# Performance work log

Measured on AMD Instinct MI355X. Metric: run time of the kernel, lower is better.

## Reference

```python
import jax, jax.numpy as jnp
import numpy as np

B, L, E, F, H, V = 64, 32, 512, 512, 1024, 10000


def setup_inputs() -> dict:
    key = jax.random.key(0)
    ks = jax.random.split(key, 20)
    def lin_w(k, out_d, in_d):
        # 4 stacked gate weights (i, f, o, c), PyTorch Linear-style scale
        s = 1.0 / np.sqrt(in_d)
        return jax.random.uniform(k, (4, out_d, in_d), jnp.float32, -s, s)
    def lin_b(k, out_d, in_d):
        s = 1.0 / np.sqrt(in_d)
        return jax.random.uniform(k, (4, out_d), jnp.float32, -s, s)
    inp = {
        "captions": jax.random.randint(ks[0], (B, L), 0, V),
        "image_features": jax.random.normal(ks[1], (B, E), jnp.float32),
        "B_emb": jax.random.normal(ks[2], (V, E), jnp.float32),
        "V_W": lin_w(ks[3], F, E), "V_b": lin_b(ks[4], F, E),
        "S_W": lin_w(ks[5], F, F), "S_b": lin_b(ks[6], F, F),
        "U_W": lin_w(ks[7], H, F), "U_b": lin_b(ks[8], H, F),
        "W_W": lin_w(ks[9], H, H), "W_b": lin_b(ks[10], H, H),
        "C_W": jax.random.uniform(ks[11], (V, H), jnp.float32, -1.0/np.sqrt(H), 1.0/np.sqrt(H)),
        "C_b": jax.random.uniform(ks[12], (V,), jnp.float32, -1.0/np.sqrt(H), 1.0/np.sqrt(H)),
        # original uses nn.init.uniform_ on fresh tensors -> U[0,1)
        "h0": jax.random.uniform(ks[13], (B, H), jnp.float32),
        "c0": jax.random.uniform(ks[14], (B, H), jnp.float32),
    }
    return inp


def reference(captions, image_features, B_emb, V_W, V_b, S_W, S_b, U_W, U_b,
              W_W, W_b, C_W, C_b, h0, c0):
    emb = B_emb[captions]                                   # [B, L, E]
    embedded = jnp.concatenate([image_features[:, None, :], emb], axis=1)  # [B, L+1, E]
    x = embedded[:, :-1, :]                                 # [B, T, E], T = L
    # input-dependent gate pre-activations (V -> S_d[mode] -> U), independent of h
    g = jnp.einsum('bte,gfe->btgf', x, V_W) + V_b           # [B, T, 4, F]
    g = jnp.einsum('btgf,gof->btgo', g, S_W) + S_b          # [B, T, 4, F]
    g = jnp.einsum('btgf,ghf->btgh', g, U_W) + U_b          # [B, T, 4, H]

    def step(carry, g_t):
        h, c = carry
        hg = jnp.einsum('bk,ghk->bgh', h, W_W) + W_b        # [B, 4, H]
        z = g_t + hg
        i_t = jax.nn.sigmoid(z[:, 0])
        f_t = jax.nn.sigmoid(z[:, 1])
        o_t = jax.nn.sigmoid(z[:, 2])
        c_tilda = jnp.tanh(z[:, 3])
        c_new = f_t * c + i_t * c_tilda
        h_new = o_t * c_new
        logits = h_new @ C_W.T + C_b                        # [B, V]
        return (h_new, c_new), logits

    _, outs = jax.lax.scan(step, (h0, c0), jnp.swapaxes(g, 0, 1))  # outs: [T, B, V]
    return jnp.swapaxes(outs, 0, 1)                         # [B, T, V]
```

## Files before the change

kernel.cpp:

```cpp
#include <hip/hip_runtime.h>
#include <hip/hip_bf16.h>

typedef __attribute__((ext_vector_type(8))) __bf16 bf16x8;
typedef __attribute__((ext_vector_type(4))) float f32x4;
typedef unsigned short ushort_t;

#define Bdim 64
#define Tdim 32
#define Edim 512
#define Fdim 512
#define Hdim 1024
#define Vdim 10000
#define SCAN_BLOCKS 64
#define CONS_BLOCKS 157

__device__ __forceinline__ float bf2f(ushort_t u) {
    unsigned int x = ((unsigned int)u) << 16;
    union { unsigned int i; float f; } c; c.i = x; return c.f;
}
__device__ __forceinline__ ushort_t f2bf(float f) {
    __hip_bfloat16 h = __float2bfloat16(f);
    union { __hip_bfloat16 h; ushort_t u; } c; c.h = h; return c.u;
}

__device__ __forceinline__ void gload_lds16(const void* g, void* l) {
    __builtin_amdgcn_global_load_lds(
        (const __attribute__((address_space(1))) unsigned int*)g,
        (__attribute__((address_space(3))) unsigned int*)l, 16, 0, 0);
}

__device__ __forceinline__ void store_short_wt(ushort_t* p, ushort_t v) {
    asm volatile("global_store_short %0, %1, off sc0 sc1"
                 : : "v"(p), "v"((unsigned int)v) : "memory");
}
__device__ __forceinline__ void store_uint_wt(unsigned int* p, unsigned int v) {
    asm volatile("global_store_dword %0, %1, off sc0 sc1"
                 : : "v"(p), "v"(v) : "memory");
}

__global__ void cvt_all(const float* __restrict__ vw, const float* __restrict__ sw,
                        const float* __restrict__ uw, const float* __restrict__ ww,
                        const float* __restrict__ cw, const float* __restrict__ h0,
                        ushort_t* __restrict__ mir, unsigned int* __restrict__ flg) {
    if (blockIdx.x == 0) {
        int4 zz = {0, 0, 0, 0};
        ((int4*)flg)[threadIdx.x * 2 + 0] = zz;
        ((int4*)flg)[threadIdx.x * 2 + 1] = zz;
    }
    long idx = ((long)blockIdx.x * blockDim.x + threadIdx.x) * 8;
    const float* src; long off;
    if      (idx <  1048576L) { src = vw; off = idx; }
    else if (idx <  2097152L) { src = sw; off = idx - 1048576L; }
    else if (idx <  4194304L) { src = uw; off = idx - 2097152L; }
    else if (idx <  8388608L) { src = ww; off = idx - 4194304L; }
    else if (idx < 18628608L) { src = cw; off = idx - 8388608L; }
    else if (idx < 18694144L) { src = h0; off = idx - 18628608L; }
    else return;
    float4 a = *(const float4*)(src + off);
    float4 b = *(const float4*)(src + off + 4);
    ushort_t o[8];
    o[0] = f2bf(a.x); o[1] = f2bf(a.y); o[2] = f2bf(a.z); o[3] = f2bf(a.w);
    o[4] = f2bf(b.x); o[5] = f2bf(b.y); o[6] = f2bf(b.z); o[7] = f2bf(b.w);
    *(int4*)(mir + idx) = *(const int4*)o;
}

__global__ void build_x(const int* __restrict__ cap,
                        const float* __restrict__ img,
                        const float* __restrict__ emb,
                        ushort_t* __restrict__ X) {
    int idx = blockIdx.x * blockDim.x + threadIdx.x;
    int row = idx >> 6;
    int c8  = (idx & 63) << 3;
    int b = row >> 5, t = row & 31;
    const float* src = (t == 0) ? (img + (size_t)b * Edim)
                                : (emb + (size_t)cap[b * Tdim + (t - 1)] * Edim);
    float4 a  = *(const float4*)(src + c8);
    float4 bb = *(const float4*)(src + c8 + 4);
    ushort_t o[8];
    o[0] = f2bf(a.x);  o[1] = f2bf(a.y);  o[2] = f2bf(a.z);  o[3] = f2bf(a.w);
    o[4] = f2bf(bb.x); o[5] = f2bf(bb.y); o[6] = f2bf(bb.z); o[7] = f2bf(bb.w);
    *(int4*)(X + (size_t)row * Edim + c8) = *(const int4*)o;
}

__launch_bounds__(256)
__global__ void gemm_bt(const ushort_t* __restrict__ A, long lda, long gsA,
                        const ushort_t* __restrict__ Bm, long ldb, long gsB,
                        void* __restrict__ Cv, long ldc, long gsC,
                        const float* __restrict__ bias, long gsBias,
                        int N, int K, int f32out, int zpack, int aswap) {
    __shared__ ushort_t As[128 * 64];
    __shared__ ushort_t Bs[128 * 64];
    int z = blockIdx.z;
    A += (size_t)z * gsA; Bm += (size_t)z * gsB; bias += (size_t)z * gsBias;

    int nx = gridDim.x, ny = gridDim.y;
    int lin = blockIdx.x + nx * blockIdx.y;
    int per_xcd = (nx * ny) >> 3;
    int l2 = (lin & 7) * per_xcd + (lin >> 3);
    int bx = l2 / ny, by = l2 % ny;

    int tid = threadIdx.x;
    int w = tid >> 6, l = tid & 63;
    int wm = (w >> 1) * 64, wn = (w & 1) * 64;
    int m0 = by * 128, n0 = bx * 128;

    int srow = tid >> 3;
    int scol = (tid & 7) << 3;

    int lane_r = l & 15;
    int lane_k = (l >> 4) << 3;

    f32x4 zero = {0.f, 0.f, 0.f, 0.f};
    f32x4 acc[4][4];
#pragma unroll
    for (int i = 0; i < 4; i++)
#pragma unroll
        for (int j = 0; j < 4; j++) acc[i][j] = zero;

    for (int k0 = 0; k0 < K; k0 += 64) {
#pragma unroll
        for (int j = 0; j < 4; j++) {
            int r = srow + j * 32;
            int pr = m0 + r;
            if (aswap) pr = ((pr & 31) << 6) + (pr >> 5);
            int sc = scol ^ ((r & 7) << 3);
            gload_lds16(A + (size_t)pr * lda + k0 + sc, &As[r * 64 + scol]);
        }
#pragma unroll
        for (int j = 0; j < 4; j++) {
            int r = srow + j * 32;
            int br = n0 + r; if (br > N - 1) br = N - 1;
            int sc = scol ^ ((r & 7) << 3);
            gload_lds16(Bm + (size_t)br * ldb + k0 + sc, &Bs[r * 64 + scol]);
        }
        __syncthreads();
#pragma unroll
        for (int kk = 0; kk < 64; kk += 32) {
            bf16x8 af[4], bfr[4];
#pragma unroll
            for (int i = 0; i < 4; i++) {
                int ar = wm + i * 16 + lane_r;
                af[i] = *(const bf16x8*)&As[ar * 64 + ((kk + lane_k) ^ ((ar & 7) << 3))];
            }
#pragma unroll
            for (int j = 0; j < 4; j++) {
                int br2 = wn + j * 16 + lane_r;
                bfr[j] = *(const bf16x8*)&Bs[br2 * 64 + ((kk + lane_k) ^ ((br2 & 7) << 3))];
            }
#pragma unroll
            for (int i = 0; i < 4; i++)
#pragma unroll
                for (int j = 0; j < 4; j++)
                    acc[i][j] = __builtin_amdgcn_mfma_f32_16x16x32_bf16(af[i], bfr[j], acc[i][j], 0, 0, 0);
        }
        __syncthreads();
    }

    int row_base = m0 + wm + ((l >> 4) << 2);
    int col_base = n0 + wn + lane_r;
#pragma unroll
    for (int j = 0; j < 4; j++) {
        int col = col_base + j * 16;
        if (col < N) {
            float bv = bias[col];
#pragma unroll
            for (int i = 0; i < 4; i++) {
#pragma unroll
                for (int r = 0; r < 4; r++) {
                    int row = row_base + i * 16 + r;
                    float v = acc[i][j][r] + bv;
                    if (zpack) {
                        int b = row >> 5, tt = row & 31;
                        size_t idx = (((size_t)(tt * 64 + (col >> 4)) * 4 + z) * 16
                                      + (col & 15)) * 64 + b;
                        ((ushort_t*)Cv)[idx] = f2bf(v);
                    } else if (f32out) {
                        ((float*)Cv)[(size_t)z * gsC + (size_t)row * ldc + col] = v;
                    } else {
                        ((ushort_t*)Cv)[(size_t)z * gsC + (size_t)row * ldc + col] = f2bf(v);
                    }
                }
            }
        }
    }
}

#define GLD(i, o) asm volatile("global_load_dwordx4 %0, %1, off offset:" o \
                               : "=v"(ab[i]) : "v"(apx))
#define CHUNK(d, n, ISSUE)                                                                   \
    do {                                                                                     \
        const int kc2 = ((d) * 32 + lane_kb) * 2;                                            \
        bf16x8 b0 = *(const bf16x8*)((const char*)Ws + ((     lane_r) * 2048 + (kc2 ^ swz)));\
        bf16x8 b1 = *(const bf16x8*)((const char*)Ws + ((16 + lane_r) * 2048 + (kc2 ^ swz)));\
        bf16x8 b2 = *(const bf16x8*)((const char*)Ws + ((32 + lane_r) * 2048 + (kc2 ^ swz)));\
        bf16x8 b3 = *(const bf16x8*)((const char*)Ws + ((48 + lane_r) * 2048 + (kc2 ^ swz)));\
        asm volatile("s_waitcnt vmcnt(" n ")");                                              \
        __builtin_amdgcn_sched_barrier(0);                                                   \
        bf16x8 av = __builtin_bit_cast(bf16x8, ab[(d) & 15]);                                \
        acc[0] = __builtin_amdgcn_mfma_f32_16x16x32_bf16(av, b0, acc[0], 0, 0, 0);           \
        acc[1] = __builtin_amdgcn_mfma_f32_16x16x32_bf16(av, b1, acc[1], 0, 0, 0);           \
        acc[2] = __builtin_amdgcn_mfma_f32_16x16x32_bf16(av, b2, acc[2], 0, 0, 0);           \
        acc[3] = __builtin_amdgcn_mfma_f32_16x16x32_bf16(av, b3, acc[3], 0, 0, 0);           \
        ISSUE;                                                                               \
    } while (0)
#define KLOOP32()                                                                            \
    int4 ab[16];                                                                             \
    GLD(0, "0");    GLD(1, "64");   GLD(2, "128");  GLD(3, "192");                           \
    GLD(4, "256");  GLD(5, "320");  GLD(6, "384");  GLD(7, "448");                           \
    GLD(8, "512");  GLD(9, "576");  GLD(10, "640"); GLD(11, "704");                          \
    GLD(12, "768"); GLD(13, "832"); GLD(14, "896"); GLD(15, "960");                          \
    CHUNK(0, "15", GLD(0, "1024"));  CHUNK(1, "15", GLD(1, "1088"));                         \
    CHUNK(2, "15", GLD(2, "1152"));  CHUNK(3, "15", GLD(3, "1216"));                         \
    CHUNK(4, "15", GLD(4, "1280"));  CHUNK(5, "15", GLD(5, "1344"));                         \
    CHUNK(6, "15", GLD(6, "1408"));  CHUNK(7, "15", GLD(7, "1472"));                         \
    CHUNK(8, "15", GLD(8, "1536"));  CHUNK(9, "15", GLD(9, "1600"));                         \
    CHUNK(10, "15", GLD(10, "1664")); CHUNK(11, "15", GLD(11, "1728"));                      \
    CHUNK(12, "15", GLD(12, "1792")); CHUNK(13, "15", GLD(13, "1856"));                      \
    CHUNK(14, "15", GLD(14, "1920")); CHUNK(15, "15", GLD(15, "1984"));                      \
    CHUNK(16, "15", (void)0); CHUNK(17, "14", (void)0);                                      \
    CHUNK(18, "13", (void)0); CHUNK(19, "12", (void)0);                                      \
    CHUNK(20, "11", (void)0); CHUNK(21, "10", (void)0);                                      \
    CHUNK(22, "9", (void)0);  CHUNK(23, "8", (void)0);                                       \
    CHUNK(24, "7", (void)0);  CHUNK(25, "6", (void)0);                                       \
    CHUNK(26, "5", (void)0);  CHUNK(27, "4", (void)0);                                       \
    CHUNK(28, "3", (void)0);  CHUNK(29, "2", (void)0);                                       \
    CHUNK(30, "1", (void)0);  CHUNK(31, "0", (void)0)

__launch_bounds__(256, 1)
__global__ void lstm_fused(const ushort_t* __restrict__ Wm,
                           const float* __restrict__ Wb,
                           const ushort_t* __restrict__ zb,
                           const ushort_t* __restrict__ h0b,
                           const float* __restrict__ c0,
                           ushort_t* __restrict__ Hbt,
                           unsigned int* __restrict__ flags,
                           const ushort_t* __restrict__ CWb,
                           const float* __restrict__ Cb,
                           float* __restrict__ out) {
    __shared__ ushort_t Ws[64 * 1024];
    int bid = blockIdx.x;
    int tid = threadIdx.x;
    int w = tid >> 6, l = tid & 63;
    int lane_r = l & 15, lane_kb = (l >> 4) << 3;

    if (bid < SCAN_BLOCKS) {
        int cg = bid;
        for (int e = tid * 8; e < 65536; e += 2048) {
            int rowl = e >> 10, ke = e & 1023;
            int g = rowl >> 4, hc = rowl & 15;
            const ushort_t* src = Wm + ((size_t)(g * Hdim + cg * 16 + hc)) * Hdim + ke;
            int dstb = rowl * 2048 + ((ke * 2) ^ ((rowl & 7) << 4));
            *(int4*)((char*)Ws + dstb) = *(const int4*)src;
        }
        int hcol = cg * 16 + lane_r;
        float wbv[4];
#pragma unroll
        for (int g = 0; g < 4; g++) wbv[g] = Wb[g * Hdim + hcol];
        int rb0 = w * 16 + ((l >> 4) << 2);
        float cst[4];
#pragma unroll
        for (int r = 0; r < 4; r++) cst[r] = c0[(size_t)(rb0 + r) * Hdim + hcol];
        __syncthreads();

        int arow = w * 16 + lane_r;
        int swz = (lane_r & 7) << 4;

        for (int t = 0; t < Tdim; t++) {
            ushort_t g3s[4][4];
            size_t zbase = ((size_t)t * 64 + cg) * 4096 + (size_t)lane_r * 64 + rb0;
#pragma unroll
            for (int g = 0; g < 4; g++)
                *(ushort4*)g3s[g] = *(const ushort4*)(zb + zbase + (size_t)g * 1024);

            if (t > 0) {
                const unsigned int* fp = flags + (size_t)(t - 1) * 64 + l;
                unsigned int v;
                do {
                    v = __hip_atomic_load(fp, __ATOMIC_RELAXED, __HIP_MEMORY_SCOPE_AGENT);
                } while (__ballot(v != 0) != 0xFFFFFFFFFFFFFFFFull);
            }
            __builtin_amdgcn_sched_barrier(0);

            const ushort_t* hp = t ? (Hbt + (size_t)(t - 1) * (Bdim * Hdim)) : h0b;
            const ushort_t* apx = hp + (size_t)arow * Hdim + lane_kb;

            f32x4 zero = {0.f, 0.f, 0.f, 0.f};
            f32x4 acc[4];
#pragma unroll
            for (int g = 0; g < 4; g++) acc[g] = zero;

            KLOOP32();

#pragma unroll
            for (int r = 0; r < 4; r++) {
                float zi = acc[0][r] + wbv[0] + bf2f(g3s[0][r]);
                float zf = acc[1][r] + wbv[1] + bf2f(g3s[1][r]);
                float zo = acc[2][r] + wbv[2] + bf2f(g3s[2][r]);
                float zc = acc[3][r] + wbv[3] + bf2f(g3s[3][r]);
                float it = __builtin_amdgcn_rcpf(1.f + __expf(-zi));
                float ft = __builtin_amdgcn_rcpf(1.f + __expf(-zf));
                float ot = __builtin_amdgcn_rcpf(1.f + __expf(-zo));
                float e2 = __expf(-2.f * zc);
                float ct = (1.f - e2) * __builtin_amdgcn_rcpf(1.f + e2);
                float cn = ft * cst[r] + it * ct;
                cst[r] = cn;
                store_short_wt(Hbt + (size_t)t * (Bdim * Hdim) + (size_t)(rb0 + r) * Hdim + hcol,
                               f2bf(ot * cn));
            }

            asm volatile("s_waitcnt vmcnt(0)" ::: "memory");
            __syncthreads();
            if (tid == 0) store_uint_wt(flags + (size_t)t * 64 + cg, 1u);
        }
    } else {
        int j = bid - SCAN_BLOCKS;
        for (int e = tid * 8; e < 65536; e += 2048) {
            int rowl = e >> 10, ke = e & 1023;
            int n = j * 64 + rowl; if (n > Vdim - 1) n = Vdim - 1;
            const ushort_t* src = CWb + (size_t)n * Hdim + ke;
            int dstb = rowl * 2048 + ((ke * 2) ^ ((rowl & 7) << 4));
            *(int4*)((char*)Ws + dstb) = *(const int4*)src;
        }
        int rb0 = w * 16 + ((l >> 4) << 2);
        int arow = w * 16 + lane_r;
        int swz = (lane_r & 7) << 4;
        float cbv[4];
#pragma unroll
        for (int g = 0; g < 4; g++) {
            int col = j * 64 + g * 16 + lane_r;
            cbv[g] = Cb[col > Vdim - 1 ? Vdim - 1 : col];
        }
        __syncthreads();

        for (int t = 0; t < Tdim; t++) {
            if (w == 0) {
                const unsigned int* fp = flags + (size_t)t * 64 + l;
                unsigned int v;
                do {
                    __builtin_amdgcn_s_sleep(8);
                    v = __hip_atomic_load(fp, __ATOMIC_RELAXED, __HIP_MEMORY_SCOPE_AGENT);
                } while (__ballot(v != 0) != 0xFFFFFFFFFFFFFFFFull);
            }
            __syncthreads();
            __builtin_amdgcn_sched_barrier(0);

            const ushort_t* apx = Hbt + (size_t)t * (Bdim * Hdim) + (size_t)arow * Hdim + lane_kb;

            f32x4 zero = {0.f, 0.f, 0.f, 0.f};
            f32x4 acc[4];
#pragma unroll
            for (int g = 0; g < 4; g++) acc[g] = zero;

            KLOOP32();

#pragma unroll
            for (int g = 0; g < 4; g++) {
                int col = j * 64 + g * 16 + lane_r;
                if (col < Vdim) {
#pragma unroll
                    for (int r = 0; r < 4; r++)
                        out[((size_t)(rb0 + r) * Tdim + t) * Vdim + col] = acc[g][r] + cbv[g];
                }
            }
        }
    }
}

extern "C" void kernel_launch(void* const* d_in, const int* in_sizes, int n_in,
                              void* d_out, int out_size, void* d_ws, size_t ws_size,
                              hipStream_t stream) {
    const int*   cap  = (const int*)d_in[0];
    const float* img  = (const float*)d_in[1];
    const float* Bemb = (const float*)d_in[2];
    const float* V_W  = (const float*)d_in[3];
    const float* V_b  = (const float*)d_in[4];
    const float* S_W  = (const float*)d_in[5];
    const float* S_b  = (const float*)d_in[6];
    const float* U_W  = (const float*)d_in[7];
    const float* U_b  = (const float*)d_in[8];
    const float* W_W  = (const float*)d_in[9];
    const float* W_b  = (const float*)d_in[10];
    const float* C_W  = (const float*)d_in[11];
    const float* C_b  = (const float*)d_in[12];
    const float* h0   = (const float*)d_in[13];
    const float* c0   = (const float*)d_in[14];

    char* ws = (char*)d_ws;
    int fused = ws_size >= (size_t)(64u) * 1024 * 1024;

    ushort_t* mir = (ushort_t*)(ws);
    ushort_t* X   = (ushort_t*)(ws + (size_t)(36u << 20));
    ushort_t* g1  = (ushort_t*)(ws + (size_t)(38u << 20));
    ushort_t *g2, *Hbt, *zbp; unsigned int* flags;
    if (fused) {
        zbp   = (ushort_t*)(ws + (size_t)(36u << 20));
        g2    = (ushort_t*)(ws + (size_t)(52u << 20));
        Hbt   = (ushort_t*)(ws + (size_t)(60u << 20));
        flags = (unsigned int*)(ws + (size_t)(36u << 20) - 16384);
    } else {
        zbp   = (ushort_t*)d_out;
        g2    = (ushort_t*)(ws + (size_t)(46u << 20));
        Hbt   = (ushort_t*)(ws + (size_t)(54u << 20));
        flags = (unsigned int*)(ws + (size_t)(58u << 20));
    }

    const ushort_t* V_Wb = mir;
    const ushort_t* S_Wb = mir + 1048576L;
    const ushort_t* U_Wb = mir + 2097152L;
    const ushort_t* W_Wb = mir + 4194304L;
    const ushort_t* C_Wb = mir + 8388608L;
    const ushort_t* h0b  = mir + 18628608L;

    cvt_all<<<9128, 256, 0, stream>>>(V_W, S_W, U_W, W_W, C_W, h0, mir, flags);
    build_x<<<512, 256, 0, stream>>>(cap, img, Bemb, X);

    gemm_bt<<<dim3(16, 16, 1), 256, 0, stream>>>(X, 512, 0, V_Wb, 512, 0,
                                                 g1, 2048, 0, V_b, 0, 2048, 512, 0, 0, 0);
    gemm_bt<<<dim3(4, 16, 4), 256, 0, stream>>>(g1, 2048, 512, S_Wb, 512, 512 * 512,
                                                g2, 2048, 512, S_b, 512, 512, 512, 0, 0, 0);
    gemm_bt<<<dim3(8, 16, 4), 256, 0, stream>>>(g2, 2048, 512, U_Wb, 512, 1024 * 512,
                                                zbp, 0, 0, U_b, 1024, 1024, 512, 0, 1, 0);
    {
        const ushort_t* a0 = W_Wb; const float* a1 = W_b; const ushort_t* a2 = zbp;
        const ushort_t* a3 = h0b;  const float* a4 = c0;  ushort_t* a5 = Hbt;
        unsigned int* a6 = flags;  const ushort_t* a7 = C_Wb; const float* a8 = C_b;
        float* a9 = (float*)d_out;
        void* sargs[10] = {(void*)&a0, (void*)&a1, (void*)&a2, (void*)&a3, (void*)&a4,
                           (void*)&a5, (void*)&a6, (void*)&a7, (void*)&a8, (void*)&a9};
        int grid = fused ? (SCAN_BLOCKS + CONS_BLOCKS) : SCAN_BLOCKS;
        hipLaunchCooperativeKernel((const void*)lstm_fused, dim3(grid), dim3(256),
                                   sargs, 0, stream);
    }
    if (!fused) {
        gemm_bt<<<dim3(79, 16, 1), 256, 0, stream>>>(Hbt, 1024, 0, C_Wb, 1024, 0,
                                                     d_out, 10000, 0, C_b, 0,
                                                     10000, 1024, 1, 0, 1);
    }
}
```

Baseline: 381.5 us.

## Convert C_W to bf16 inside fused consumer blocks and use single done flag

In the fused path the vocabulary projection weights are no longer converted to bf16 by the pre-pass kernel. Each consumer block now loads its fp32 slice of C_W and converts it while filling shared memory, which shrinks cvt_all and removes the extra global write and re-read of the bf16 mirror. Consumers also stop polling all 64 per-block flags and instead spin on one per-step 'done' word, written by scan block 0 after it sees all flags for that step. This cuts polling traffic but adds one hop of latency before consumers start each step.

```diff
diff --git a/kernel.cpp b/kernel.cpp
--- a/kernel.cpp
+++ b/kernel.cpp
@@ -40,12 +40,12 @@
 
 __global__ void cvt_all(const float* __restrict__ vw, const float* __restrict__ sw,
                         const float* __restrict__ uw, const float* __restrict__ ww,
-                        const float* __restrict__ cw, const float* __restrict__ h0,
+                        const float* __restrict__ h0, const float* __restrict__ cw,
                         ushort_t* __restrict__ mir, unsigned int* __restrict__ flg) {
     if (blockIdx.x == 0) {
         int4 zz = {0, 0, 0, 0};
-        ((int4*)flg)[threadIdx.x * 2 + 0] = zz;
-        ((int4*)flg)[threadIdx.x * 2 + 1] = zz;
+#pragma unroll
+        for (int q = 0; q < 4; q++) ((int4*)flg)[threadIdx.x * 4 + q] = zz;
     }
     long idx = ((long)blockIdx.x * blockDim.x + threadIdx.x) * 8;
     const float* src; long off;
@@ -53,8 +53,8 @@
     else if (idx <  2097152L) { src = sw; off = idx - 1048576L; }
     else if (idx <  4194304L) { src = uw; off = idx - 2097152L; }
     else if (idx <  8388608L) { src = ww; off = idx - 4194304L; }
-    else if (idx < 18628608L) { src = cw; off = idx - 8388608L; }
-    else if (idx < 18694144L) { src = h0; off = idx - 18628608L; }
+    else if (idx <  8454144L) { src = h0; off = idx - 8388608L; }
+    else if (idx < 18694144L) { src = cw; off = idx - 8454144L; }
     else return;
     float4 a = *(const float4*)(src + off);
     float4 b = *(const float4*)(src + off + 4);
@@ -234,10 +234,11 @@
                            const float* __restrict__ c0,
                            ushort_t* __restrict__ Hbt,
                            unsigned int* __restrict__ flags,
-                           const ushort_t* __restrict__ CWb,
+                           const float* __restrict__ CWf,
                            const float* __restrict__ Cb,
                            float* __restrict__ out) {
     __shared__ ushort_t Ws[64 * 1024];
+    unsigned int* done = flags + 2048;
     int bid = blockIdx.x;
     int tid = threadIdx.x;
     int w = tid >> 6, l = tid & 63;
@@ -278,6 +279,7 @@
                 do {
                     v = __hip_atomic_load(fp, __ATOMIC_RELAXED, __HIP_MEMORY_SCOPE_AGENT);
                 } while (__ballot(v != 0) != 0xFFFFFFFFFFFFFFFFull);
+                if (cg == 0 && tid == 0) store_uint_wt(done + (t - 1), 1u);
             }
             __builtin_amdgcn_sched_barrier(0);
 
@@ -312,14 +314,27 @@
             __syncthreads();
             if (tid == 0) store_uint_wt(flags + (size_t)t * 64 + cg, 1u);
         }
+        if (cg == 0) {
+            const unsigned int* fp = flags + (size_t)31 * 64 + l;
+            unsigned int v;
+            do {
+                v = __hip_atomic_load(fp, __ATOMIC_RELAXED, __HIP_MEMORY_SCOPE_AGENT);
+            } while (__ballot(v != 0) != 0xFFFFFFFFFFFFFFFFull);
+            if (tid == 0) store_uint_wt(done + 31, 1u);
+        }
     } else {
         int j = bid - SCAN_BLOCKS;
         for (int e = tid * 8; e < 65536; e += 2048) {
             int rowl = e >> 10, ke = e & 1023;
             int n = j * 64 + rowl; if (n > Vdim - 1) n = Vdim - 1;
-            const ushort_t* src = CWb + (size_t)n * Hdim + ke;
+            const float* src = CWf + (size_t)n * Hdim + ke;
+            float4 a = *(const float4*)(src);
+            float4 b = *(const float4*)(src + 4);
+            ushort_t o[8];
+            o[0] = f2bf(a.x); o[1] = f2bf(a.y); o[2] = f2bf(a.z); o[3] = f2bf(a.w);
+            o[4] = f2bf(b.x); o[5] = f2bf(b.y); o[6] = f2bf(b.z); o[7] = f2bf(b.w);
             int dstb = rowl * 2048 + ((ke * 2) ^ ((rowl & 7) << 4));
-            *(int4*)((char*)Ws + dstb) = *(const int4*)src;
+            *(int4*)((char*)Ws + dstb) = *(const int4*)o;
         }
         int rb0 = w * 16 + ((l >> 4) << 2);
         int arow = w * 16 + lane_r;
@@ -334,12 +349,12 @@
 
         for (int t = 0; t < Tdim; t++) {
             if (w == 0) {
-                const unsigned int* fp = flags + (size_t)t * 64 + l;
+                const unsigned int* dp = done + t;
                 unsigned int v;
                 do {
-                    __builtin_amdgcn_s_sleep(8);
-                    v = __hip_atomic_load(fp, __ATOMIC_RELAXED, __HIP_MEMORY_SCOPE_AGENT);
-                } while (__ballot(v != 0) != 0xFFFFFFFFFFFFFFFFull);
+                    __builtin_amdgcn_s_sleep(4);
+                    v = __hip_atomic_load(dp, __ATOMIC_RELAXED, __HIP_MEMORY_SCOPE_AGENT);
+                } while (v == 0);
             }
             __syncthreads();
             __builtin_amdgcn_sched_barrier(0);
@@ -408,10 +423,10 @@
     const ushort_t* S_Wb = mir + 1048576L;
     const ushort_t* U_Wb = mir + 2097152L;
     const ushort_t* W_Wb = mir + 4194304L;
-    const ushort_t* C_Wb = mir + 8388608L;
-    const ushort_t* h0b  = mir + 18628608L;
-
-    cvt_all<<<9128, 256, 0, stream>>>(V_W, S_W, U_W, W_W, C_W, h0, mir, flags);
+    const ushort_t* h0b  = mir + 8388608L;
+    const ushort_t* C_Wb = mir + 8454144L;
+
+    cvt_all<<<fused ? 4128 : 9128, 256, 0, stream>>>(V_W, S_W, U_W, W_W, h0, C_W, mir, flags);
     build_x<<<512, 256, 0, stream>>>(cap, img, Bemb, X);
 
     gemm_bt<<<dim3(16, 16, 1), 256, 0, stream>>>(X, 512, 0, V_Wb, 512, 0,
@@ -423,7 +438,7 @@
     {
         const ushort_t* a0 = W_Wb; const float* a1 = W_b; const ushort_t* a2 = zbp;
         const ushort_t* a3 = h0b;  const float* a4 = c0;  ushort_t* a5 = Hbt;
-        unsigned int* a6 = flags;  const ushort_t* a7 = C_Wb; const float* a8 = C_b;
+        unsigned int* a6 = flags;  const float* a7 = C_W; const float* a8 = C_b;
         float* a9 = (float*)d_out;
         void* sargs[10] = {(void*)&a0, (void*)&a1, (void*)&a2, (void*)&a3, (void*)&a4,
                            (void*)&a5, (void*)&a6, (void*)&a7, (void*)&a8, (void*)&a9};
```

Result: faster. 332.2 us (-12.9%).
